# Kernel optimization log

Hardware: AMD Instinct MI355X
Metric: run time of the kernel (lower is better)

The kernel has to match this reference:

```python
import jax, jax.numpy as jnp
import numpy as np

N_NODES = 50000
N_EDGES = 800000
IN_DIM, HID_DIM, OUT_DIM = 256, 128, 64


def gcn_conv(x, edge_index, W, b):
    """PyG GCNConv: out = D^{-1/2} (A + I) D^{-1/2} (x @ W) + b."""
    n = x.shape[0]
    loops = jnp.arange(n, dtype=edge_index.dtype)
    src = jnp.concatenate([edge_index[0], loops])  # message source j
    dst = jnp.concatenate([edge_index[1], loops])  # aggregation target i
    ones = jnp.ones(src.shape[0], dtype=x.dtype)
    deg = jax.ops.segment_sum(ones, dst, num_segments=n)  # >= 1 (self-loops)
    dinv = jax.lax.rsqrt(deg)
    norm = dinv[src] * dinv[dst]                    # [E+N]
    h = x @ W                                       # [N, out] GEMM first (PyG order)
    msg = h[src] * norm[:, None]                    # gather + scale
    out = jax.ops.segment_sum(msg, dst, num_segments=n)  # scatter-add
    return out + b


def setup_inputs() -> dict:
    key = jax.random.key(0)
    k1, k2, k3, k4, k5 = jax.random.split(key, 5)
    x = jax.random.normal(k1, (N_NODES, IN_DIM), dtype=jnp.float32)
    edge_index = jax.random.randint(k2, (2, N_EDGES), 0, N_NODES, dtype=jnp.int64)
    # Glorot-ish init for weights, zero bias (PyG defaults)
    W1 = jax.random.normal(k3, (IN_DIM, HID_DIM), dtype=jnp.float32) / np.sqrt(IN_DIM)
    b1 = jnp.zeros((HID_DIM,), dtype=jnp.float32)
    W2 = jax.random.normal(k4, (HID_DIM, OUT_DIM), dtype=jnp.float32) / np.sqrt(HID_DIM)
    b2 = jnp.zeros((OUT_DIM,), dtype=jnp.float32)
    return {"x": x, "edge_index": edge_index, "W1": W1, "b1": b1, "W2": W2, "b2": b2}


def reference(x, edge_index, W1, b1, W2, b2):
    h = jax.nn.relu(gcn_conv(x, edge_index, W1, b1))
    return gcn_conv(h, edge_index, W2, b2)
```

## Files before the change

kernel.cpp:

```cpp
#include <hip/hip_runtime.h>

#define N_NODES 50000
#define N_EDGES 800000
#define IN_DIM 256
#define HID_DIM 128
#define OUT_DIM 64
#define CAP 64

#define K_BINS 256
#define NPB 196
#define BINCAP 4096
#define CHUNK 4096
#define N_BINWG 196

typedef __bf16 bf16x8 __attribute__((ext_vector_type(8)));
typedef float f32x4 __attribute__((ext_vector_type(4)));
typedef unsigned short u16x8 __attribute__((ext_vector_type(8)));
typedef unsigned short ushort_t;
typedef unsigned int uint_t;

__device__ __forceinline__ ushort_t f2bf(float f) {
    uint_t u = __float_as_uint(f);
    return (ushort_t)((u + 0x7fffu + ((u >> 16) & 1u)) >> 16);
}
__device__ __forceinline__ float bf_lo(uint_t u) { return __uint_as_float(u << 16); }
__device__ __forceinline__ float bf_hi(uint_t u) { return __uint_as_float(u & 0xffff0000u); }

__global__ __launch_bounds__(256) void k_init(const float* __restrict__ W1,
                                              ushort_t* __restrict__ w1t,
                                              const float* __restrict__ W2,
                                              ushort_t* __restrict__ w2t) {
    const int bid = blockIdx.x;
    const int t = threadIdx.x;
    if (bid < 128) {
        int id = bid * 256 + t;
        int k = id >> 7, c = id & 127;
        w1t[c * IN_DIM + k] = f2bf(W1[id]);
    } else {
        int id = (bid - 128) * 256 + t;
        int k = id >> 6, c = id & 63;
        w2t[c * HID_DIM + k] = f2bf(W2[id]);
    }
}

__global__ __launch_bounds__(256) void k_bin(const int* __restrict__ srcs,
                                             const int* __restrict__ dsts,
                                             int* __restrict__ bin_cur,
                                             uint_t* __restrict__ binbuf) {
    __shared__ int lcnt[K_BINS];
    __shared__ int lbase[K_BINS];
    const int t = threadIdx.x;
    lcnt[t] = 0;
    __syncthreads();
    const int start = blockIdx.x * CHUNK;
    int b_[16]; int p_[16]; uint_t rec_[16];
#pragma unroll
    for (int k = 0; k < 16; ++k) {
        int e = start + t + k * 256;
        bool ok = (e < N_EDGES);
        int d = ok ? dsts[e] : 0;
        int s = ok ? srcs[e] : 0;
        int b = d / NPB;
        b_[k] = ok ? b : -1;
        p_[k] = ok ? atomicAdd(&lcnt[b], 1) : 0;
        rec_[k] = (uint_t)s | ((uint_t)(d - b * NPB) << 16);
    }
    __syncthreads();
    lbase[t] = atomicAdd(&bin_cur[t], lcnt[t]);
    __syncthreads();
#pragma unroll
    for (int k = 0; k < 16; ++k) {
        if (b_[k] >= 0) {
            int pos = lbase[b_[k]] + p_[k];
            if (pos < BINCAP) binbuf[(size_t)b_[k] * BINCAP + pos] = rec_[k];
        }
    }
}

__global__ __launch_bounds__(256) void k_fill(const int* __restrict__ bin_cur,
                                              const uint_t* __restrict__ binbuf,
                                              ushort_t* __restrict__ es,
                                              float* __restrict__ dinv,
                                              int* __restrict__ ndeg) {
    __shared__ int cnt[NPB];
    __shared__ __align__(16) ushort_t pay[NPB][CAP];
    const int b = blockIdx.x, t = threadIdx.x;
    if (t < NPB) cnt[t] = 0;
    __syncthreads();
    const int n = min(bin_cur[b], BINCAP);
    const uint_t* rec = binbuf + (size_t)b * BINCAP;
    for (int e = t; e < n; e += 256) {
        uint_t r = rec[e];
        int dl = r >> 16;
        int p = atomicAdd(&cnt[dl], 1);
        if (p < CAP) pay[dl][p] = (ushort_t)(r & 0xffffu);
    }
    __syncthreads();
    uint4* gdst = (uint4*)(es + (size_t)b * NPB * CAP);
    const uint4* lsrc = (const uint4*)&pay[0][0];
    for (int i = t; i < NPB * CAP / 8; i += 256) gdst[i] = lsrc[i];
    if (t < NPB) {
        int node = b * NPB + t;
        if (node < N_NODES) {
            int deg = cnt[t];
            dinv[node] = rsqrtf((float)(deg + 1));
            ndeg[node] = min(deg, CAP);
        }
    }
}

__global__ __launch_bounds__(64) void k_gemm1(const float* __restrict__ x,
                                              const ushort_t* __restrict__ w1t,
                                              ushort_t* __restrict__ hb) {
    const int lane = threadIdx.x;
    const int l15 = lane & 15, quad = lane >> 4;
    const int row = blockIdx.x * 16 + l15;
    f32x4 acc[8];
#pragma unroll
    for (int n = 0; n < 8; ++n) acc[n] = (f32x4){0.f, 0.f, 0.f, 0.f};
    const float* xrow = x + (size_t)row * IN_DIM + quad * 8;
    const ushort_t* wbase = w1t + quad * 8;
#pragma unroll
    for (int t = 0; t < 8; ++t) {
        const float4* xp = (const float4*)(xrow + t * 32);
        float4 f0 = xp[0], f1 = xp[1];
        u16x8 au;
        au[0] = f2bf(f0.x); au[1] = f2bf(f0.y); au[2] = f2bf(f0.z); au[3] = f2bf(f0.w);
        au[4] = f2bf(f1.x); au[5] = f2bf(f1.y); au[6] = f2bf(f1.z); au[7] = f2bf(f1.w);
        bf16x8 a = __builtin_bit_cast(bf16x8, au);
#pragma unroll
        for (int n = 0; n < 8; ++n) {
            bf16x8 b = *(const bf16x8*)(wbase + (n * 16 + l15) * IN_DIM + t * 32);
            acc[n] = __builtin_amdgcn_mfma_f32_16x16x32_bf16(a, b, acc[n], 0, 0, 0);
        }
    }
    ushort_t* hrow = hb + ((size_t)blockIdx.x * 16 + quad * 4) * HID_DIM + l15;
#pragma unroll
    for (int n = 0; n < 8; ++n)
#pragma unroll
        for (int r = 0; r < 4; ++r)
            hrow[(size_t)r * HID_DIM + n * 16] = f2bf(acc[n][r]);
}

__global__ __launch_bounds__(256) void k_agg1(const ushort_t* __restrict__ hb,
                                              const int* __restrict__ ndeg,
                                              const float* __restrict__ dinv,
                                              const ushort_t* __restrict__ es,
                                              const float* __restrict__ b,
                                              ushort_t* __restrict__ hrelu) {
    const int i = blockIdx.x * 4 + (threadIdx.x >> 6);
    const int lane = threadIdx.x & 63;
    const int half = lane >> 5;
    const int c = lane & 31;
    const float dv = dinv[i];
    const int n = ndeg[i];
    int   sj = 0;
    float nmj = 0.f;
    if (lane < n) {
        sj = (int)__builtin_nontemporal_load(&es[i * CAP + lane]);
        nmj = dinv[sj] * dv;
    }
    float a0 = 0.f, a1 = 0.f, a2 = 0.f, a3 = 0.f;
    int j = 0;
    for (; j + 16 <= n; j += 16) {
        int   s0 = __shfl(sj, j + half),      s1 = __shfl(sj, j + 2 + half);
        int   s2 = __shfl(sj, j + 4 + half),  s3 = __shfl(sj, j + 6 + half);
        int   s4 = __shfl(sj, j + 8 + half),  s5 = __shfl(sj, j + 10 + half);
        int   s6 = __shfl(sj, j + 12 + half), s7 = __shfl(sj, j + 14 + half);
        float m0 = __shfl(nmj, j + half),      m1 = __shfl(nmj, j + 2 + half);
        float m2 = __shfl(nmj, j + 4 + half),  m3 = __shfl(nmj, j + 6 + half);
        float m4 = __shfl(nmj, j + 8 + half),  m5 = __shfl(nmj, j + 10 + half);
        float m6 = __shfl(nmj, j + 12 + half), m7 = __shfl(nmj, j + 14 + half);
        uint2 v0 = *(const uint2*)(hb + (size_t)s0 * HID_DIM + 4 * c);
        uint2 v1 = *(const uint2*)(hb + (size_t)s1 * HID_DIM + 4 * c);
        uint2 v2 = *(const uint2*)(hb + (size_t)s2 * HID_DIM + 4 * c);
        uint2 v3 = *(const uint2*)(hb + (size_t)s3 * HID_DIM + 4 * c);
        uint2 v4 = *(const uint2*)(hb + (size_t)s4 * HID_DIM + 4 * c);
        uint2 v5 = *(const uint2*)(hb + (size_t)s5 * HID_DIM + 4 * c);
        uint2 v6 = *(const uint2*)(hb + (size_t)s6 * HID_DIM + 4 * c);
        uint2 v7 = *(const uint2*)(hb + (size_t)s7 * HID_DIM + 4 * c);
        a0 += bf_lo(v0.x) * m0 + bf_lo(v1.x) * m1 + bf_lo(v2.x) * m2 + bf_lo(v3.x) * m3
            + bf_lo(v4.x) * m4 + bf_lo(v5.x) * m5 + bf_lo(v6.x) * m6 + bf_lo(v7.x) * m7;
        a1 += bf_hi(v0.x) * m0 + bf_hi(v1.x) * m1 + bf_hi(v2.x) * m2 + bf_hi(v3.x) * m3
            + bf_hi(v4.x) * m4 + bf_hi(v5.x) * m5 + bf_hi(v6.x) * m6 + bf_hi(v7.x) * m7;
        a2 += bf_lo(v0.y) * m0 + bf_lo(v1.y) * m1 + bf_lo(v2.y) * m2 + bf_lo(v3.y) * m3
            + bf_lo(v4.y) * m4 + bf_lo(v5.y) * m5 + bf_lo(v6.y) * m6 + bf_lo(v7.y) * m7;
        a3 += bf_hi(v0.y) * m0 + bf_hi(v1.y) * m1 + bf_hi(v2.y) * m2 + bf_hi(v3.y) * m3
            + bf_hi(v4.y) * m4 + bf_hi(v5.y) * m5 + bf_hi(v6.y) * m6 + bf_hi(v7.y) * m7;
    }
    for (; j < n; j += 2) {
        int   s = __shfl(sj, j + half);
        float m = __shfl(nmj, j + half);
        uint2 v = *(const uint2*)(hb + (size_t)s * HID_DIM + 4 * c);
        a0 += bf_lo(v.x) * m; a1 += bf_hi(v.x) * m;
        a2 += bf_lo(v.y) * m; a3 += bf_hi(v.y) * m;
    }
    a0 += __shfl_xor(a0, 32); a1 += __shfl_xor(a1, 32);
    a2 += __shfl_xor(a2, 32); a3 += __shfl_xor(a3, 32);
    if (lane < 32) {
        uint2 u = *(const uint2*)(hb + (size_t)i * HID_DIM + 4 * c);
        const float dvv = dv * dv;
        float r0 = a0 + bf_lo(u.x) * dvv + b[4 * c];
        float r1 = a1 + bf_hi(u.x) * dvv + b[4 * c + 1];
        float r2 = a2 + bf_lo(u.y) * dvv + b[4 * c + 2];
        float r3 = a3 + bf_hi(u.y) * dvv + b[4 * c + 3];
        r0 = fmaxf(r0, 0.f); r1 = fmaxf(r1, 0.f);
        r2 = fmaxf(r2, 0.f); r3 = fmaxf(r3, 0.f);
        uint2 o;
        o.x = ((uint_t)f2bf(r1) << 16) | f2bf(r0);
        o.y = ((uint_t)f2bf(r3) << 16) | f2bf(r2);
        *(uint2*)(hrelu + (size_t)i * HID_DIM + 4 * c) = o;
    }
}

__global__ __launch_bounds__(64) void k_gemm2(const ushort_t* __restrict__ hrelu,
                                              const ushort_t* __restrict__ w2t,
                                              ushort_t* __restrict__ h2) {
    const int lane = threadIdx.x;
    const int l15 = lane & 15, quad = lane >> 4;
    const int row = blockIdx.x * 16 + l15;
    f32x4 acc[4];
#pragma unroll
    for (int n = 0; n < 4; ++n) acc[n] = (f32x4){0.f, 0.f, 0.f, 0.f};
    const ushort_t* arow = hrelu + (size_t)row * HID_DIM + quad * 8;
    const ushort_t* wbase = w2t + quad * 8;
#pragma unroll
    for (int t = 0; t < 4; ++t) {
        bf16x8 a = *(const bf16x8*)(arow + t * 32);
#pragma unroll
        for (int n = 0; n < 4; ++n) {
            bf16x8 b = *(const bf16x8*)(wbase + (n * 16 + l15) * HID_DIM + t * 32);
            acc[n] = __builtin_amdgcn_mfma_f32_16x16x32_bf16(a, b, acc[n], 0, 0, 0);
        }
    }
    ushort_t* orow = h2 + ((size_t)blockIdx.x * 16 + quad * 4) * OUT_DIM + l15;
#pragma unroll
    for (int n = 0; n < 4; ++n)
#pragma unroll
        for (int r = 0; r < 4; ++r)
            orow[(size_t)r * OUT_DIM + n * 16] = f2bf(acc[n][r]);
}

__global__ __launch_bounds__(256) void k_agg2(const ushort_t* __restrict__ h2,
                                              const int* __restrict__ ndeg,
                                              const float* __restrict__ dinv,
                                              const ushort_t* __restrict__ es,
                                              const float* __restrict__ b,
                                              float* __restrict__ out) {
    const int i = blockIdx.x * 4 + (threadIdx.x >> 6);
    const int lane = threadIdx.x & 63;
    const int half = lane >> 5;
    const int c = lane & 31;
    const float dv = dinv[i];
    const int n = ndeg[i];
    int   sj = 0;
    float nmj = 0.f;
    if (lane < n) {
        sj = (int)__builtin_nontemporal_load(&es[i * CAP + lane]);
        nmj = dinv[sj] * dv;
    }
    float a0 = 0.f, a1 = 0.f;
    int j = 0;
    for (; j + 16 <= n; j += 16) {
        int   s0 = __shfl(sj, j + half),      s1 = __shfl(sj, j + 2 + half);
        int   s2 = __shfl(sj, j + 4 + half),  s3 = __shfl(sj, j + 6 + half);
        int   s4 = __shfl(sj, j + 8 + half),  s5 = __shfl(sj, j + 10 + half);
        int   s6 = __shfl(sj, j + 12 + half), s7 = __shfl(sj, j + 14 + half);
        float m0 = __shfl(nmj, j + half),      m1 = __shfl(nmj, j + 2 + half);
        float m2 = __shfl(nmj, j + 4 + half),  m3 = __shfl(nmj, j + 6 + half);
        float m4 = __shfl(nmj, j + 8 + half),  m5 = __shfl(nmj, j + 10 + half);
        float m6 = __shfl(nmj, j + 12 + half), m7 = __shfl(nmj, j + 14 + half);
        uint_t v0 = *(const uint_t*)(h2 + (size_t)s0 * OUT_DIM + 2 * c);
        uint_t v1 = *(const uint_t*)(h2 + (size_t)s1 * OUT_DIM + 2 * c);
        uint_t v2 = *(const uint_t*)(h2 + (size_t)s2 * OUT_DIM + 2 * c);
        uint_t v3 = *(const uint_t*)(h2 + (size_t)s3 * OUT_DIM + 2 * c);
        uint_t v4 = *(const uint_t*)(h2 + (size_t)s4 * OUT_DIM + 2 * c);
        uint_t v5 = *(const uint_t*)(h2 + (size_t)s5 * OUT_DIM + 2 * c);
        uint_t v6 = *(const uint_t*)(h2 + (size_t)s6 * OUT_DIM + 2 * c);
        uint_t v7 = *(const uint_t*)(h2 + (size_t)s7 * OUT_DIM + 2 * c);
        a0 += bf_lo(v0) * m0 + bf_lo(v1) * m1 + bf_lo(v2) * m2 + bf_lo(v3) * m3
            + bf_lo(v4) * m4 + bf_lo(v5) * m5 + bf_lo(v6) * m6 + bf_lo(v7) * m7;
        a1 += bf_hi(v0) * m0 + bf_hi(v1) * m1 + bf_hi(v2) * m2 + bf_hi(v3) * m3
            + bf_hi(v4) * m4 + bf_hi(v5) * m5 + bf_hi(v6) * m6 + bf_hi(v7) * m7;
    }
    for (; j < n; j += 2) {
        int   s = __shfl(sj, j + half);
        float m = __shfl(nmj, j + half);
        uint_t v = *(const uint_t*)(h2 + (size_t)s * OUT_DIM + 2 * c);
        a0 += bf_lo(v) * m;
        a1 += bf_hi(v) * m;
    }
    a0 += __shfl_xor(a0, 32);
    a1 += __shfl_xor(a1, 32);
    if (lane < 32) {
        uint_t u = *(const uint_t*)(h2 + (size_t)i * OUT_DIM + 2 * c);
        float2 r;
        r.x = a0 + bf_lo(u) * dv * dv + b[2 * c];
        r.y = a1 + bf_hi(u) * dv * dv + b[2 * c + 1];
        *(float2*)(out + (size_t)i * OUT_DIM + 2 * c) = r;
    }
}

extern "C" void kernel_launch(void* const* d_in, const int* in_sizes, int n_in,
                              void* d_out, int out_size, void* d_ws, size_t ws_size,
                              hipStream_t stream) {
    const float* x   = (const float*)d_in[0];
    const int*   ei  = (const int*)d_in[1];
    const float* W1  = (const float*)d_in[2];
    const float* b1  = (const float*)d_in[3];
    const float* W2  = (const float*)d_in[4];
    const float* b2  = (const float*)d_in[5];
    float* out = (float*)d_out;

    const int* srcs = ei;
    const int* dsts = ei + N_EDGES;

    char* ws = (char*)d_ws;
    size_t o = 0;
    auto alloc = [&](size_t bytes) { void* p = ws + o; o = (o + bytes + 511) & ~size_t(511); return p; };
    int*      bin_cur = (int*)   alloc(K_BINS * 4);
    float*    dinv  = (float*)   alloc(N_NODES * 4);
    int*      ndeg  = (int*)     alloc(N_NODES * 4);
    ushort_t* es    = (ushort_t*)alloc((size_t)K_BINS * NPB * CAP * 2);
    uint_t*   binbuf= (uint_t*)  alloc((size_t)K_BINS * BINCAP * 4);
    ushort_t* w1t   = (ushort_t*)alloc((size_t)IN_DIM * HID_DIM * 2);
    ushort_t* w2t   = (ushort_t*)alloc((size_t)HID_DIM * OUT_DIM * 2);
    ushort_t* hb    = (ushort_t*)alloc((size_t)N_NODES * HID_DIM * 2);
    ushort_t* hrelu = (ushort_t*)alloc((size_t)N_NODES * HID_DIM * 2);
    ushort_t* h2    = (ushort_t*)alloc((size_t)N_NODES * OUT_DIM * 2);

    hipMemsetAsync(bin_cur, 0, K_BINS * 4, stream);
    k_init  <<<160, 256, 0, stream>>>(W1, w1t, W2, w2t);
    k_bin   <<<N_BINWG, 256, 0, stream>>>(srcs, dsts, bin_cur, binbuf);
    k_fill  <<<K_BINS, 256, 0, stream>>>(bin_cur, binbuf, es, dinv, ndeg);
    k_gemm1 <<<N_NODES / 16, 64, 0, stream>>>(x, w1t, hb);
    k_agg1  <<<N_NODES / 4, 256, 0, stream>>>(hb, ndeg, dinv, es, b1, hrelu);
    k_gemm2 <<<N_NODES / 16, 64, 0, stream>>>(hrelu, w2t, h2);
    k_agg2  <<<N_NODES / 4, 256, 0, stream>>>(h2, ndeg, dinv, es, b2, out);
}
```

Baseline: 220.9 us.

## Merge weight-init with binning and CSR fill with GEMM1 into combined launches

The weight transpose/convert blocks and the edge-binning blocks now share one launch, and the per-bin CSR fill blocks share a launch with the first GEMM. Both pairs are independent, so merging them removes two kernel launches and their serialization gaps. The two GEMMs also move from 64-thread blocks to 256-thread blocks of four waves with row bounds guards. Binning uses smaller chunks with more workgroups. The fill and GEMM blocks in the merged launch are heterogeneous, and the fill block's large shared allocation may limit how many blocks fit on a CU alongside the GEMM blocks.

```diff
diff --git a/kernel.cpp b/kernel.cpp
--- a/kernel.cpp
+++ b/kernel.cpp
@@ -10,8 +10,10 @@
 #define K_BINS 256
 #define NPB 196
 #define BINCAP 4096
-#define CHUNK 4096
-#define N_BINWG 196
+#define CHUNK 2048
+#define N_BINWG 391
+#define N_WBLK 160
+#define N_G1BLK 782
 
 typedef __bf16 bf16x8 __attribute__((ext_vector_type(8)));
 typedef float f32x4 __attribute__((ext_vector_type(4)));
@@ -26,36 +28,36 @@
 __device__ __forceinline__ float bf_lo(uint_t u) { return __uint_as_float(u << 16); }
 __device__ __forceinline__ float bf_hi(uint_t u) { return __uint_as_float(u & 0xffff0000u); }
 
-__global__ __launch_bounds__(256) void k_init(const float* __restrict__ W1,
-                                              ushort_t* __restrict__ w1t,
-                                              const float* __restrict__ W2,
-                                              ushort_t* __restrict__ w2t) {
+__global__ __launch_bounds__(256) void k_binit(const float* __restrict__ W1,
+                                               ushort_t* __restrict__ w1t,
+                                               const float* __restrict__ W2,
+                                               ushort_t* __restrict__ w2t,
+                                               const int* __restrict__ srcs,
+                                               const int* __restrict__ dsts,
+                                               int* __restrict__ bin_cur,
+                                               uint_t* __restrict__ binbuf) {
     const int bid = blockIdx.x;
     const int t = threadIdx.x;
-    if (bid < 128) {
-        int id = bid * 256 + t;
-        int k = id >> 7, c = id & 127;
-        w1t[c * IN_DIM + k] = f2bf(W1[id]);
-    } else {
-        int id = (bid - 128) * 256 + t;
-        int k = id >> 6, c = id & 63;
-        w2t[c * HID_DIM + k] = f2bf(W2[id]);
-    }
-}
-
-__global__ __launch_bounds__(256) void k_bin(const int* __restrict__ srcs,
-                                             const int* __restrict__ dsts,
-                                             int* __restrict__ bin_cur,
-                                             uint_t* __restrict__ binbuf) {
+    if (bid < N_WBLK) {
+        if (bid < 128) {
+            int id = bid * 256 + t;
+            int k = id >> 7, c = id & 127;
+            w1t[c * IN_DIM + k] = f2bf(W1[id]);
+        } else {
+            int id = (bid - 128) * 256 + t;
+            int k = id >> 6, c = id & 63;
+            w2t[c * HID_DIM + k] = f2bf(W2[id]);
+        }
+        return;
+    }
     __shared__ int lcnt[K_BINS];
     __shared__ int lbase[K_BINS];
-    const int t = threadIdx.x;
     lcnt[t] = 0;
     __syncthreads();
-    const int start = blockIdx.x * CHUNK;
-    int b_[16]; int p_[16]; uint_t rec_[16];
-#pragma unroll
-    for (int k = 0; k < 16; ++k) {
+    const int start = (bid - N_WBLK) * CHUNK;
+    int b_[8]; int p_[8]; uint_t rec_[8];
+#pragma unroll
+    for (int k = 0; k < 8; ++k) {
         int e = start + t + k * 256;
         bool ok = (e < N_EDGES);
         int d = ok ? dsts[e] : 0;
@@ -69,7 +71,7 @@
     lbase[t] = atomicAdd(&bin_cur[t], lcnt[t]);
     __syncthreads();
 #pragma unroll
-    for (int k = 0; k < 16; ++k) {
+    for (int k = 0; k < 8; ++k) {
         if (b_[k] >= 0) {
             int pos = lbase[b_[k]] + p_[k];
             if (pos < BINCAP) binbuf[(size_t)b_[k] * BINCAP + pos] = rec_[k];
@@ -77,52 +79,57 @@
     }
 }
 
-__global__ __launch_bounds__(256) void k_fill(const int* __restrict__ bin_cur,
-                                              const uint_t* __restrict__ binbuf,
-                                              ushort_t* __restrict__ es,
-                                              float* __restrict__ dinv,
-                                              int* __restrict__ ndeg) {
-    __shared__ int cnt[NPB];
-    __shared__ __align__(16) ushort_t pay[NPB][CAP];
-    const int b = blockIdx.x, t = threadIdx.x;
-    if (t < NPB) cnt[t] = 0;
-    __syncthreads();
-    const int n = min(bin_cur[b], BINCAP);
-    const uint_t* rec = binbuf + (size_t)b * BINCAP;
-    for (int e = t; e < n; e += 256) {
-        uint_t r = rec[e];
-        int dl = r >> 16;
-        int p = atomicAdd(&cnt[dl], 1);
-        if (p < CAP) pay[dl][p] = (ushort_t)(r & 0xffffu);
-    }
-    __syncthreads();
-    uint4* gdst = (uint4*)(es + (size_t)b * NPB * CAP);
-    const uint4* lsrc = (const uint4*)&pay[0][0];
-    for (int i = t; i < NPB * CAP / 8; i += 256) gdst[i] = lsrc[i];
-    if (t < NPB) {
-        int node = b * NPB + t;
-        if (node < N_NODES) {
-            int deg = cnt[t];
-            dinv[node] = rsqrtf((float)(deg + 1));
-            ndeg[node] = min(deg, CAP);
-        }
-    }
-}
-
-__global__ __launch_bounds__(64) void k_gemm1(const float* __restrict__ x,
-                                              const ushort_t* __restrict__ w1t,
-                                              ushort_t* __restrict__ hb) {
-    const int lane = threadIdx.x;
+__global__ __launch_bounds__(256) void k_fillg1(const int* __restrict__ bin_cur,
+                                                const uint_t* __restrict__ binbuf,
+                                                ushort_t* __restrict__ es,
+                                                float* __restrict__ dinv,
+                                                int* __restrict__ ndeg,
+                                                const float* __restrict__ x,
+                                                const ushort_t* __restrict__ w1t,
+                                                ushort_t* __restrict__ hb) {
+    const int bid = blockIdx.x;
+    const int t = threadIdx.x;
+    if (bid < K_BINS) {
+        __shared__ int cnt[NPB];
+        __shared__ __align__(16) ushort_t pay[NPB][CAP];
+        const int b = bid;
+        if (t < NPB) cnt[t] = 0;
+        __syncthreads();
+        const int n = min(bin_cur[b], BINCAP);
+        const uint_t* rec = binbuf + (size_t)b * BINCAP;
+        for (int e = t; e < n; e += 256) {
+            uint_t r = rec[e];
+            int dl = r >> 16;
+            int p = atomicAdd(&cnt[dl], 1);
+            if (p < CAP) pay[dl][p] = (ushort_t)(r & 0xffffu);
+        }
+        __syncthreads();
+        uint4* gdst = (uint4*)(es + (size_t)b * NPB * CAP);
+        const uint4* lsrc = (const uint4*)&pay[0][0];
+        for (int i = t; i < NPB * CAP / 8; i += 256) gdst[i] = lsrc[i];
+        if (t < NPB) {
+            int node = b * NPB + t;
+            if (node < N_NODES) {
+                int deg = cnt[t];
+                dinv[node] = rsqrtf((float)(deg + 1));
+                ndeg[node] = min(deg, CAP);
+            }
+        }
+        return;
+    }
+    const int wave = t >> 6;
+    const int lane = t & 63;
     const int l15 = lane & 15, quad = lane >> 4;
-    const int row = blockIdx.x * 16 + l15;
+    const int tbase = (bid - K_BINS) * 64 + wave * 16;
+    const int row = min(tbase + l15, N_NODES - 1);
     f32x4 acc[8];
 #pragma unroll
     for (int n = 0; n < 8; ++n) acc[n] = (f32x4){0.f, 0.f, 0.f, 0.f};
     const float* xrow = x + (size_t)row * IN_DIM + quad * 8;
     const ushort_t* wbase = w1t + quad * 8;
 #pragma unroll
-    for (int t = 0; t < 8; ++t) {
-        const float4* xp = (const float4*)(xrow + t * 32);
+    for (int tk = 0; tk < 8; ++tk) {
+        const float4* xp = (const float4*)(xrow + tk * 32);
         float4 f0 = xp[0], f1 = xp[1];
         u16x8 au;
         au[0] = f2bf(f0.x); au[1] = f2bf(f0.y); au[2] = f2bf(f0.z); au[3] = f2bf(f0.w);
@@ -130,16 +137,18 @@
         bf16x8 a = __builtin_bit_cast(bf16x8, au);
 #pragma unroll
         for (int n = 0; n < 8; ++n) {
-            bf16x8 b = *(const bf16x8*)(wbase + (n * 16 + l15) * IN_DIM + t * 32);
+            bf16x8 b = *(const bf16x8*)(wbase + (n * 16 + l15) * IN_DIM + tk * 32);
             acc[n] = __builtin_amdgcn_mfma_f32_16x16x32_bf16(a, b, acc[n], 0, 0, 0);
         }
     }
-    ushort_t* hrow = hb + ((size_t)blockIdx.x * 16 + quad * 4) * HID_DIM + l15;
+    const int row0 = tbase + quad * 4;
+    ushort_t* hrow = hb + (size_t)row0 * HID_DIM + l15;
 #pragma unroll
     for (int n = 0; n < 8; ++n)
 #pragma unroll
         for (int r = 0; r < 4; ++r)
-            hrow[(size_t)r * HID_DIM + n * 16] = f2bf(acc[n][r]);
+            if (row0 + r < N_NODES)
+                hrow[(size_t)r * HID_DIM + n * 16] = f2bf(acc[n][r]);
 }
 
 __global__ __launch_bounds__(256) void k_agg1(const ushort_t* __restrict__ hb,
@@ -213,32 +222,37 @@
     }
 }
 
-__global__ __launch_bounds__(64) void k_gemm2(const ushort_t* __restrict__ hrelu,
-                                              const ushort_t* __restrict__ w2t,
-                                              ushort_t* __restrict__ h2) {
-    const int lane = threadIdx.x;
+__global__ __launch_bounds__(256) void k_gemm2(const ushort_t* __restrict__ hrelu,
+                                               const ushort_t* __restrict__ w2t,
+                                               ushort_t* __restrict__ h2) {
+    const int t = threadIdx.x;
+    const int wave = t >> 6;
+    const int lane = t & 63;
     const int l15 = lane & 15, quad = lane >> 4;
-    const int row = blockIdx.x * 16 + l15;
+    const int tbase = blockIdx.x * 64 + wave * 16;
+    const int row = min(tbase + l15, N_NODES - 1);
     f32x4 acc[4];
 #pragma unroll
     for (int n = 0; n < 4; ++n) acc[n] = (f32x4){0.f, 0.f, 0.f, 0.f};
     const ushort_t* arow = hrelu + (size_t)row * HID_DIM + quad * 8;
     const ushort_t* wbase = w2t + quad * 8;
 #pragma unroll
-    for (int t = 0; t < 4; ++t) {
-        bf16x8 a = *(const bf16x8*)(arow + t * 32);
+    for (int tk = 0; tk < 4; ++tk) {
+        bf16x8 a = *(const bf16x8*)(arow + tk * 32);
 #pragma unroll
         for (int n = 0; n < 4; ++n) {
-            bf16x8 b = *(const bf16x8*)(wbase + (n * 16 + l15) * HID_DIM + t * 32);
+            bf16x8 b = *(const bf16x8*)(wbase + (n * 16 + l15) * HID_DIM + tk * 32);
             acc[n] = __builtin_amdgcn_mfma_f32_16x16x32_bf16(a, b, acc[n], 0, 0, 0);
         }
     }
-    ushort_t* orow = h2 + ((size_t)blockIdx.x * 16 + quad * 4) * OUT_DIM + l15;
+    const int row0 = tbase + quad * 4;
+    ushort_t* orow = h2 + (size_t)row0 * OUT_DIM + l15;
 #pragma unroll
     for (int n = 0; n < 4; ++n)
 #pragma unroll
         for (int r = 0; r < 4; ++r)
-            orow[(size_t)r * OUT_DIM + n * 16] = f2bf(acc[n][r]);
+            if (row0 + r < N_NODES)
+                orow[(size_t)r * OUT_DIM + n * 16] = f2bf(acc[n][r]);
 }
 
 __global__ __launch_bounds__(256) void k_agg2(const ushort_t* __restrict__ h2,
@@ -330,11 +344,9 @@
     ushort_t* h2    = (ushort_t*)alloc((size_t)N_NODES * OUT_DIM * 2);
 
     hipMemsetAsync(bin_cur, 0, K_BINS * 4, stream);
-    k_init  <<<160, 256, 0, stream>>>(W1, w1t, W2, w2t);
-    k_bin   <<<N_BINWG, 256, 0, stream>>>(srcs, dsts, bin_cur, binbuf);
-    k_fill  <<<K_BINS, 256, 0, stream>>>(bin_cur, binbuf, es, dinv, ndeg);
-    k_gemm1 <<<N_NODES / 16, 64, 0, stream>>>(x, w1t, hb);
+    k_binit <<<N_WBLK + N_BINWG, 256, 0, stream>>>(W1, w1t, W2, w2t, srcs, dsts, bin_cur, binbuf);
+    k_fillg1<<<K_BINS + N_G1BLK, 256, 0, stream>>>(bin_cur, binbuf, es, dinv, ndeg, x, w1t, hb);
     k_agg1  <<<N_NODES / 4, 256, 0, stream>>>(hb, ndeg, dinv, es, b1, hrelu);
-    k_gemm2 <<<N_NODES / 16, 64, 0, stream>>>(hrelu, w2t, h2);
+    k_gemm2 <<<N_G1BLK, 256, 0, stream>>>(hrelu, w2t, h2);
     k_agg2  <<<N_NODES / 4, 256, 0, stream>>>(h2, ndeg, dinv, es, b2, out);
 }
```

After: 219.9 us. About the same (-0.5%).
